# Performance work log

Hardware: AMD Instinct MI355X
Metric: run time of the kernel (lower is better)

Reference implementation:

```python
import jax, jax.numpy as jnp
import numpy as np

N_CLASS = 29   # len('SE?abcdefghijklmnopqrstuvwxyz')
N_HIDDEN = 128


def _rnn(x, h0, Wih, Whh, bih, bhh):
    """PyTorch nn.RNN (tanh, 1 layer, batch_first) semantics.
    x: [B,T,I], h0: [B,H]. Returns (outputs [B,T,H], h_T [B,H]).
    h_t = tanh(x_t @ Wih^T + bih + h_{t-1} @ Whh^T + bhh)
    """
    # Precompute input projection for all timesteps (batched GEMM).
    xp = jnp.einsum('bti,hi->bth', x, Wih) + (bih + bhh)  # [B,T,H]

    def step(h, xt):  # xt: [B,H]
        h_new = jnp.tanh(xt + h @ Whh.T)
        return h_new, h_new

    hT, hs = jax.lax.scan(step, h0, jnp.swapaxes(xp, 0, 1))  # scan over T
    return jnp.swapaxes(hs, 0, 1), hT


def setup_inputs() -> dict:
    key = jax.random.key(0)
    ks = jax.random.split(key, 12)
    B, T = 2048, 256
    s = 1.0 / np.sqrt(N_HIDDEN)  # PyTorch RNN/Linear init scale
    inp = {
        'encoder_input': jax.random.normal(ks[0], (B, T, N_CLASS), jnp.float32),
        'encoder_hidden': jnp.zeros((1, B, N_HIDDEN), jnp.float32),
        'decoder_input': jax.random.normal(ks[1], (B, T, N_CLASS), jnp.float32),
        'enc_Wih': jax.random.uniform(ks[2], (N_HIDDEN, N_CLASS), jnp.float32, -s, s),
        'enc_Whh': jax.random.uniform(ks[3], (N_HIDDEN, N_HIDDEN), jnp.float32, -s, s),
        'enc_bih': jax.random.uniform(ks[4], (N_HIDDEN,), jnp.float32, -s, s),
        'enc_bhh': jax.random.uniform(ks[5], (N_HIDDEN,), jnp.float32, -s, s),
        'dec_Wih': jax.random.uniform(ks[6], (N_HIDDEN, N_CLASS), jnp.float32, -s, s),
        'dec_Whh': jax.random.uniform(ks[7], (N_HIDDEN, N_HIDDEN), jnp.float32, -s, s),
        'dec_bih': jax.random.uniform(ks[8], (N_HIDDEN,), jnp.float32, -s, s),
        'dec_bhh': jax.random.uniform(ks[9], (N_HIDDEN,), jnp.float32, -s, s),
        'fc_W': jax.random.uniform(ks[10], (N_CLASS, N_HIDDEN), jnp.float32, -s, s),
        'fc_b': jax.random.uniform(ks[11], (N_CLASS,), jnp.float32, -s, s),
    }
    return inp


def reference(encoder_input, encoder_hidden, decoder_input,
              enc_Wih, enc_Whh, enc_bih, enc_bhh,
              dec_Wih, dec_Whh, dec_bih, dec_bhh,
              fc_W, fc_b):
    h0 = encoder_hidden[0]                                   # [B,H]
    _, h_t = _rnn(encoder_input, h0, enc_Wih, enc_Whh, enc_bih, enc_bhh)
    dec_out, _ = _rnn(decoder_input, h_t, dec_Wih, dec_Whh, dec_bih, dec_bhh)  # [B,T,H]
    return jnp.einsum('bth,ch->btc', dec_out, fc_W) + fc_b   # [B,T,n_class]
```

## Files before the change

### kernel.cpp

```cpp
#include <hip/hip_runtime.h>
#include <math.h>

#define TT 256
#define NI 29
#define HH 128
#define NC 29
#define ROWS 16
#define PSTR 168

typedef _Float16 f16x8 __attribute__((ext_vector_type(8)));
typedef _Float16 f16x4 __attribute__((ext_vector_type(4)));
typedef float f32x4 __attribute__((ext_vector_type(4)));

__device__ __forceinline__ float fast_tanh(float x) {
    float ax = fabsf(x);
    float e = __builtin_amdgcn_exp2f(ax * -2.885390081777927f);
    float r = (1.0f - e) * __builtin_amdgcn_rcpf(1.0f + e);
    return copysignf(r, x);
}

template <int IS_DEC>
__launch_bounds__(512, 1)
__global__ void rnn_mfma(const float* __restrict__ xin,
                         const float* __restrict__ h0p, long h0s,
                         const float* __restrict__ Wih,
                         const float* __restrict__ Whh,
                         const float* __restrict__ bih,
                         const float* __restrict__ bhh,
                         const float* __restrict__ fcW,
                         const float* __restrict__ fcb,
                         float* __restrict__ out)
{
    __shared__ __align__(16) _Float16 planes[2][2][ROWS][PSTR];

    const int tid  = threadIdx.x;
    const int lane = tid & 63;
    const int w    = tid >> 6;
    const int m    = lane & 15;
    const int g    = lane >> 4;
    const int b0   = blockIdx.x * ROWS;

    const int jr = 16 * w + m;
    f16x8 Aw[5];
#pragma unroll
    for (int s = 0; s < 4; ++s) {
        const float* src = Whh + jr * HH + 32 * s + 8 * g;
        float4 v0 = *(const float4*)src;
        float4 v1 = *(const float4*)(src + 4);
        f16x8 a;
        a[0] = (_Float16)v0.x; a[1] = (_Float16)v0.y;
        a[2] = (_Float16)v0.z; a[3] = (_Float16)v0.w;
        a[4] = (_Float16)v1.x; a[5] = (_Float16)v1.y;
        a[6] = (_Float16)v1.z; a[7] = (_Float16)v1.w;
        Aw[s] = a;
    }
    {
        f16x8 a;
#pragma unroll
        for (int e = 0; e < 8; ++e) {
            int i = 8 * g + e;
            float v = (i < NI) ? Wih[jr * NI + i] : 0.f;
            a[e] = (_Float16)v;
        }
        Aw[4] = a;
    }
    float bias[4];
#pragma unroll
    for (int q = 0; q < 4; ++q)
        bias[q] = bih[16 * w + 4 * g + q] + bhh[16 * w + 4 * g + q];

    const int fcw = w - 6;
    f16x8 Afc[4];
    float fcbv[4];
    if (IS_DEC && fcw >= 0) {
        int c = 16 * fcw + m;
#pragma unroll
        for (int s = 0; s < 4; ++s) {
            f16x8 a;
#pragma unroll
            for (int e = 0; e < 8; ++e) {
                int k = 32 * s + 8 * g + e;
                a[e] = (c < NC) ? (_Float16)fcW[c * HH + k] : (_Float16)0.f;
            }
            Afc[s] = a;
        }
#pragma unroll
        for (int q = 0; q < 4; ++q) {
            int c2 = 16 * fcw + 4 * g + q;
            fcbv[q] = (c2 < NC) ? fcb[c2] : 0.f;
        }
    }

    if (tid < 2 * ROWS * (32 - NI)) {
        int k = tid % (32 - NI);
        int b = (tid / (32 - NI)) % ROWS;
        int d = tid / ((32 - NI) * ROWS);
        planes[d][0][b][HH + NI + k] = (_Float16)0.f;
    }

    {
        int b  = (tid * 4) >> 7;
        int i0 = (tid * 4) & 127;
        const float* hr = h0p + (long)(b0 + b) * h0s + i0;
        float4 v = *(const float4*)hr;
        float vv[4] = {v.x, v.y, v.z, v.w};
        f16x4 hi, lo;
#pragma unroll
        for (int e = 0; e < 4; ++e) {
            _Float16 h = (_Float16)vv[e];
            hi[e] = h;
            lo[e] = (_Float16)(vv[e] - (float)h);
        }
        *(f16x4*)&planes[0][0][b][i0] = hi;
        *(f16x4*)&planes[0][1][b][i0] = lo;
    }
    if (tid < ROWS * NI) {
        int b = tid / NI, i = tid % NI;
        planes[0][0][b][HH + i] = (_Float16)xin[((long)(b0 + b) * TT) * NI + i];
    }
    __syncthreads();

    for (int t = 0; t < TT; ++t) {
        const int cur = t & 1, nxt = cur ^ 1;

        f16x8 Bhi[5], Blo[4];
#pragma unroll
        for (int s = 0; s < 5; ++s)
            Bhi[s] = *(const f16x8*)&planes[cur][0][m][32 * s + 8 * g];
#pragma unroll
        for (int s = 0; s < 4; ++s)
            Blo[s] = *(const f16x8*)&planes[cur][1][m][32 * s + 8 * g];

        f32x4 acc0 = {0.f, 0.f, 0.f, 0.f};
        f32x4 acc1 = {0.f, 0.f, 0.f, 0.f};
#pragma unroll
        for (int s = 0; s < 4; ++s) {
            acc0 = __builtin_amdgcn_mfma_f32_16x16x32_f16(Aw[s], Bhi[s], acc0, 0, 0, 0);
            acc1 = __builtin_amdgcn_mfma_f32_16x16x32_f16(Aw[s], Blo[s], acc1, 0, 0, 0);
        }
        acc0 = __builtin_amdgcn_mfma_f32_16x16x32_f16(Aw[4], Bhi[4], acc0, 0, 0, 0);

        if (IS_DEC && fcw >= 0 && t > 0) {
            f32x4 fa = {0.f, 0.f, 0.f, 0.f};
#pragma unroll
            for (int s = 0; s < 4; ++s)
                fa = __builtin_amdgcn_mfma_f32_16x16x32_f16(Afc[s], Bhi[s], fa, 0, 0, 0);
#pragma unroll
            for (int q = 0; q < 4; ++q) {
                int c = 16 * fcw + 4 * g + q;
                if (c < NC)
                    out[((long)(b0 + m) * TT + (t - 1)) * NC + c] = fa[q] + fcbv[q];
            }
        }

        {
            f16x4 hi, lo;
#pragma unroll
            for (int q = 0; q < 4; ++q) {
                float h = fast_tanh(acc0[q] + acc1[q] + bias[q]);
                _Float16 hh = (_Float16)h;
                hi[q] = hh;
                lo[q] = (_Float16)(h - (float)hh);
            }
            *(f16x4*)&planes[nxt][0][m][16 * w + 4 * g] = hi;
            *(f16x4*)&planes[nxt][1][m][16 * w + 4 * g] = lo;
        }

        if (t + 1 < TT && tid < ROWS * NI) {
            int b = tid / NI, i = tid % NI;
            planes[nxt][0][b][HH + i] =
                (_Float16)xin[((long)(b0 + b) * TT + (t + 1)) * NI + i];
        }
        __syncthreads();
    }

    if (IS_DEC) {
        if (fcw >= 0) {
            f16x8 Bh[4];
#pragma unroll
            for (int s = 0; s < 4; ++s)
                Bh[s] = *(const f16x8*)&planes[0][0][m][32 * s + 8 * g];
            f32x4 fa = {0.f, 0.f, 0.f, 0.f};
#pragma unroll
            for (int s = 0; s < 4; ++s)
                fa = __builtin_amdgcn_mfma_f32_16x16x32_f16(Afc[s], Bh[s], fa, 0, 0, 0);
#pragma unroll
            for (int q = 0; q < 4; ++q) {
                int c = 16 * fcw + 4 * g + q;
                if (c < NC)
                    out[((long)(b0 + m) * TT + (TT - 1)) * NC + c] = fa[q] + fcbv[q];
            }
        }
    } else {
        int b  = (tid * 4) >> 7;
        int i0 = (tid * 4) & 127;
        float4 v;
        v.x = (float)planes[0][0][b][i0 + 0] + (float)planes[0][1][b][i0 + 0];
        v.y = (float)planes[0][0][b][i0 + 1] + (float)planes[0][1][b][i0 + 1];
        v.z = (float)planes[0][0][b][i0 + 2] + (float)planes[0][1][b][i0 + 2];
        v.w = (float)planes[0][0][b][i0 + 3] + (float)planes[0][1][b][i0 + 3];
        *(float4*)(out + (long)(b0 + b) * TT * NC + i0) = v;
    }
}

extern "C" void kernel_launch(void* const* d_in, const int* in_sizes, int n_in,
                              void* d_out, int out_size, void* d_ws, size_t ws_size,
                              hipStream_t stream) {
    const float* enc_in  = (const float*)d_in[0];
    const float* enc_h0  = (const float*)d_in[1];
    const float* dec_in  = (const float*)d_in[2];
    const float* enc_Wih = (const float*)d_in[3];
    const float* enc_Whh = (const float*)d_in[4];
    const float* enc_bih = (const float*)d_in[5];
    const float* enc_bhh = (const float*)d_in[6];
    const float* dec_Wih = (const float*)d_in[7];
    const float* dec_Whh = (const float*)d_in[8];
    const float* dec_bih = (const float*)d_in[9];
    const float* dec_bhh = (const float*)d_in[10];
    const float* fc_W    = (const float*)d_in[11];
    const float* fc_b    = (const float*)d_in[12];
    float* out = (float*)d_out;

    dim3 grid(2048 / ROWS), block(512);

    rnn_mfma<0><<<grid, block, 0, stream>>>(enc_in, enc_h0, (long)HH,
                                            enc_Wih, enc_Whh, enc_bih, enc_bhh,
                                            nullptr, nullptr, out);
    rnn_mfma<1><<<grid, block, 0, stream>>>(dec_in, out, (long)TT * NC,
                                            dec_Wih, dec_Whh, dec_bih, dec_bhh,
                                            fc_W, fc_b, out);
}
```

Measured before the change: 452.3 us.

## Prefetch inputs into registers two steps ahead and split MFMA accumulation chains

```diff
diff --git a/kernel.cpp b/kernel.cpp
--- a/kernel.cpp
+++ b/kernel.cpp
@@ -6,7 +6,7 @@
 #define HH 128
 #define NC 29
 #define ROWS 16
-#define PSTR 168
+#define PSTR 136
 
 typedef _Float16 f16x8 __attribute__((ext_vector_type(8)));
 typedef _Float16 f16x4 __attribute__((ext_vector_type(4)));
@@ -18,6 +18,67 @@
     float r = (1.0f - e) * __builtin_amdgcn_rcpf(1.0f + e);
     return copysignf(r, x);
 }
+
+__device__ __forceinline__ void load_x(const float* p, int g, float4& a, float4& b) {
+    a = *(const float4*)p;
+    if (g < 3) {
+        b = *(const float4*)(p + 4);
+    } else {
+        b.x = p[4];
+        b.y = 0.f; b.z = 0.f; b.w = 0.f;
+    }
+}
+
+#define MFMA16(A, B, C) __builtin_amdgcn_mfma_f32_16x16x32_f16((A), (B), (C), 0, 0, 0)
+
+#define STEP(CUR, X0, X1, TV)                                                 \
+  {                                                                           \
+    f16x8 bx;                                                                 \
+    bx[0] = (_Float16)X0.x; bx[1] = (_Float16)X0.y;                           \
+    bx[2] = (_Float16)X0.z; bx[3] = (_Float16)X0.w;                           \
+    bx[4] = (_Float16)X1.x; bx[5] = (_Float16)X1.y;                           \
+    bx[6] = (_Float16)X1.z; bx[7] = (_Float16)X1.w;                           \
+    if ((TV) + 2 < TT) load_x(xrow + ((TV) + 2) * NI, g, X0, X1);             \
+    f16x8 Bhi[4], Blo[4];                                                     \
+    _Pragma("unroll") for (int s = 0; s < 4; ++s)                             \
+      Bhi[s] = *(const f16x8*)&planes[CUR][0][m][32 * s + 8 * g];             \
+    _Pragma("unroll") for (int s = 0; s < 4; ++s)                             \
+      Blo[s] = *(const f16x8*)&planes[CUR][1][m][32 * s + 8 * g];             \
+    f32x4 c0 = {0.f,0.f,0.f,0.f}, c1 = {0.f,0.f,0.f,0.f};                     \
+    f32x4 c2 = {0.f,0.f,0.f,0.f}, c3 = {0.f,0.f,0.f,0.f};                     \
+    c0 = MFMA16(Aw[4], bx, c0);                                               \
+    c1 = MFMA16(Aw[1], Bhi[1], c1);                                           \
+    c2 = MFMA16(Aw[2], Bhi[2], c2);                                           \
+    c3 = MFMA16(Aw[3], Bhi[3], c3);                                           \
+    c0 = MFMA16(Aw[0], Bhi[0], c0);                                           \
+    c1 = MFMA16(Aw[1], Blo[1], c1);                                           \
+    c2 = MFMA16(Aw[2], Blo[2], c2);                                           \
+    c3 = MFMA16(Aw[3], Blo[3], c3);                                           \
+    c0 = MFMA16(Aw[0], Blo[0], c0);                                           \
+    if (IS_DEC && fcw >= 0 && (TV) > 0) {                                     \
+      f32x4 f0 = {0.f,0.f,0.f,0.f}, f1 = {0.f,0.f,0.f,0.f};                   \
+      f0 = MFMA16(Afc[0], Bhi[0], f0);                                        \
+      f1 = MFMA16(Afc[1], Bhi[1], f1);                                        \
+      f0 = MFMA16(Afc[2], Bhi[2], f0);                                        \
+      f1 = MFMA16(Afc[3], Bhi[3], f1);                                        \
+      _Pragma("unroll") for (int q = 0; q < 4; ++q) {                         \
+        int c = 16 * fcw + 4 * g + q;                                         \
+        if (c < NC)                                                           \
+          out[((long)(b0 + m) * TT + ((TV) - 1)) * NC + c] =                  \
+              f0[q] + f1[q] + fcbv[q];                                        \
+      }                                                                       \
+    }                                                                         \
+    f16x4 hhi, hlo;                                                           \
+    _Pragma("unroll") for (int q = 0; q < 4; ++q) {                           \
+      float hv = fast_tanh(c0[q] + c1[q] + c2[q] + c3[q] + bias[q]);          \
+      _Float16 hh = (_Float16)hv;                                             \
+      hhi[q] = hh;                                                            \
+      hlo[q] = (_Float16)(hv - (float)hh);                                    \
+    }                                                                         \
+    *(f16x4*)&planes[CUR ^ 1][0][m][16 * w + 4 * g] = hhi;                    \
+    *(f16x4*)&planes[CUR ^ 1][1][m][16 * w + 4 * g] = hlo;                    \
+    __syncthreads();                                                          \
+  }
 
 template <int IS_DEC>
 __launch_bounds__(512, 1)
@@ -91,13 +152,6 @@
         }
     }
 
-    if (tid < 2 * ROWS * (32 - NI)) {
-        int k = tid % (32 - NI);
-        int b = (tid / (32 - NI)) % ROWS;
-        int d = tid / ((32 - NI) * ROWS);
-        planes[d][0][b][HH + NI + k] = (_Float16)0.f;
-    }
-
     {
         int b  = (tid * 4) >> 7;
         int i0 = (tid * 4) & 127;
@@ -114,81 +168,36 @@
         *(f16x4*)&planes[0][0][b][i0] = hi;
         *(f16x4*)&planes[0][1][b][i0] = lo;
     }
-    if (tid < ROWS * NI) {
-        int b = tid / NI, i = tid % NI;
-        planes[0][0][b][HH + i] = (_Float16)xin[((long)(b0 + b) * TT) * NI + i];
-    }
+
+    const float* xrow = xin + ((long)(b0 + m) * TT) * NI + 8 * g;
+    float4 xa0, xa1, xb0, xb1;
+    load_x(xrow + 0 * NI, g, xa0, xa1);
+    load_x(xrow + 1 * NI, g, xb0, xb1);
+
     __syncthreads();
 
-    for (int t = 0; t < TT; ++t) {
-        const int cur = t & 1, nxt = cur ^ 1;
-
-        f16x8 Bhi[5], Blo[4];
-#pragma unroll
-        for (int s = 0; s < 5; ++s)
-            Bhi[s] = *(const f16x8*)&planes[cur][0][m][32 * s + 8 * g];
-#pragma unroll
-        for (int s = 0; s < 4; ++s)
-            Blo[s] = *(const f16x8*)&planes[cur][1][m][32 * s + 8 * g];
-
-        f32x4 acc0 = {0.f, 0.f, 0.f, 0.f};
-        f32x4 acc1 = {0.f, 0.f, 0.f, 0.f};
-#pragma unroll
-        for (int s = 0; s < 4; ++s) {
-            acc0 = __builtin_amdgcn_mfma_f32_16x16x32_f16(Aw[s], Bhi[s], acc0, 0, 0, 0);
-            acc1 = __builtin_amdgcn_mfma_f32_16x16x32_f16(Aw[s], Blo[s], acc1, 0, 0, 0);
-        }
-        acc0 = __builtin_amdgcn_mfma_f32_16x16x32_f16(Aw[4], Bhi[4], acc0, 0, 0, 0);
-
-        if (IS_DEC && fcw >= 0 && t > 0) {
-            f32x4 fa = {0.f, 0.f, 0.f, 0.f};
+    for (int t = 0; t < TT; t += 2) {
+        STEP(0, xa0, xa1, t);
+        STEP(1, xb0, xb1, t + 1);
+    }
+
+    if (IS_DEC) {
+        if (fcw >= 0) {
+            f16x8 Bh[4];
 #pragma unroll
             for (int s = 0; s < 4; ++s)
-                fa = __builtin_amdgcn_mfma_f32_16x16x32_f16(Afc[s], Bhi[s], fa, 0, 0, 0);
+                Bh[s] = *(const f16x8*)&planes[0][0][m][32 * s + 8 * g];
+            f32x4 f0 = {0.f,0.f,0.f,0.f}, f1 = {0.f,0.f,0.f,0.f};
+            f0 = MFMA16(Afc[0], Bh[0], f0);
+            f1 = MFMA16(Afc[1], Bh[1], f1);
+            f0 = MFMA16(Afc[2], Bh[2], f0);
+            f1 = MFMA16(Afc[3], Bh[3], f1);
 #pragma unroll
             for (int q = 0; q < 4; ++q) {
                 int c = 16 * fcw + 4 * g + q;
                 if (c < NC)
-                    out[((long)(b0 + m) * TT + (t - 1)) * NC + c] = fa[q] + fcbv[q];
-            }
-        }
-
-        {
-            f16x4 hi, lo;
-#pragma unroll
-            for (int q = 0; q < 4; ++q) {
-                float h = fast_tanh(acc0[q] + acc1[q] + bias[q]);
-                _Float16 hh = (_Float16)h;
-                hi[q] = hh;
-                lo[q] = (_Float16)(h - (float)hh);
-            }
-            *(f16x4*)&planes[nxt][0][m][16 * w + 4 * g] = hi;
-            *(f16x4*)&planes[nxt][1][m][16 * w + 4 * g] = lo;
-        }
-
-        if (t + 1 < TT && tid < ROWS * NI) {
-            int b = tid / NI, i = tid % NI;
-            planes[nxt][0][b][HH + i] =
-                (_Float16)xin[((long)(b0 + b) * TT + (t + 1)) * NI + i];
-        }
-        __syncthreads();
-    }
-
-    if (IS_DEC) {
-        if (fcw >= 0) {
-            f16x8 Bh[4];
-#pragma unroll
-            for (int s = 0; s < 4; ++s)
-                Bh[s] = *(const f16x8*)&planes[0][0][m][32 * s + 8 * g];
-            f32x4 fa = {0.f, 0.f, 0.f, 0.f};
-#pragma unroll
-            for (int s = 0; s < 4; ++s)
-                fa = __builtin_amdgcn_mfma_f32_16x16x32_f16(Afc[s], Bh[s], fa, 0, 0, 0);
-#pragma unroll
-            for (int q = 0; q < 4; ++q) {
-                int c = 16 * fcw + 4 * g + q;
-                if (c < NC)
-                    out[((long)(b0 + m) * TT + (TT - 1)) * NC + c] = fa[q] + fcbv[q];
+                    out[((long)(b0 + m) * TT + (TT - 1)) * NC + c] =
+                        f0[q] + f1[q] + fcbv[q];
             }
         }
     } else {
```

Result: slower. 610.2 us (+34.9%).
